# Kernel tuning notes

Hardware: AMD Instinct MI355X
Metric: run time of the kernel (lower is better)

## Reference

```python
import jax, jax.numpy as jnp
import numpy as np

B, S, SV = 4, 2048, 50
QF = KF = VF = E = 1024
SCALE = np.float32(np.power(KF, 0.5))


def setup_inputs() -> dict:
    key = jax.random.key(0)
    ks = jax.random.split(key, 8)
    s = 0.02
    return {
        "Q": jax.random.normal(ks[0], (B, S, QF), dtype=jnp.float32),
        "K": jax.random.normal(ks[1], (B, S, KF), dtype=jnp.float32),
        "V": jax.random.normal(ks[2], (B, SV, VF), dtype=jnp.float32),
        # weights stored [in, out] so forward is x @ W (== torch Linear with weight.T)
        "W_Q": jax.random.normal(ks[3], (QF, E), dtype=jnp.float32) * s,
        "W_K": jax.random.normal(ks[4], (KF, E), dtype=jnp.float32) * s,
        "W_v": jax.random.normal(ks[5], (E, E), dtype=jnp.float32) * s,
        "W_vq": jax.random.normal(ks[6], (SV, E), dtype=jnp.float32) * s,
        "W_vk": jax.random.normal(ks[7], (SV, E), dtype=jnp.float32) * s,
    }


def reference(Q, K, V, W_Q, W_K, W_v, W_vq, W_vk):
    # mode == 'mode2', dropout=None (inference path)
    q = jnp.tanh(Q) @ W_Q          # [B,S,E]
    k = jnp.tanh(K) @ W_K          # [B,S,E]
    v = jnp.tanh(V) @ W_v          # [B,SV,E]

    qk = jnp.einsum('bse,bte->bst', q, k) / SCALE   # [B,S,S]
    vq = jnp.einsum('bse,bve->bsv', q, v) / SCALE   # [B,S,SV]
    vk = jnp.einsum('bse,bve->bsv', k, v) / SCALE   # [B,S,SV]

    f = jax.nn.softmax(qk, axis=-1)                 # [B,S,S]
    g = 1.0 - f

    q2 = jnp.einsum('bst,bte->bse', f, q) + vq @ W_vq
    k2 = jnp.einsum('bst,bte->bse', g, k) + vk @ W_vk

    Q_out = jnp.einsum('bst,bte->bse', f, q2)
    K_out = jnp.einsum('bst,bte->bse', g, k2)
    return (Q_out, K_out, f)
```

## Files before the change

### kernel.cpp

```cpp
#include <hip/hip_runtime.h>
#include <cstdint>
#include <cstddef>

typedef __bf16 bf16_t;
typedef __bf16 bf16x4 __attribute__((ext_vector_type(4)));
typedef __bf16 bf16x8 __attribute__((ext_vector_type(8)));
typedef float floatx4 __attribute__((ext_vector_type(4)));

#define B_ 4
#define S_ 2048
#define E_ 1024
#define SV_ 50
#define SVP_ 64
#define BSE_ ((long)B_ * S_ * E_)

__device__ __forceinline__ void async_copy16(const bf16_t* g, bf16_t* l) {
  __builtin_amdgcn_global_load_lds(
      (const __attribute__((address_space(1))) void*)g,
      (__attribute__((address_space(3))) void*)l, 16, 0, 0);
}

__global__ __launch_bounds__(256) void tanh2_k(const float* __restrict__ Q,
                                               const float* __restrict__ Kin,
                                               bf16_t* __restrict__ out) {
  long i4 = ((long)blockIdx.x * 256 + threadIdx.x) * 4;
  const long n = (long)B_ * S_ * E_;
  const float* src = (i4 < n) ? (Q + i4) : (Kin + (i4 - n));
  float4 x = *(const float4*)src;
  bf16x4 o;
  o[0] = (bf16_t)tanhf(x.x);
  o[1] = (bf16_t)tanhf(x.y);
  o[2] = (bf16_t)tanhf(x.z);
  o[3] = (bf16_t)tanhf(x.w);
  *(bf16x4*)&out[i4] = o;
}

__global__ __launch_bounds__(256) void tanh_vpad_k(const float* __restrict__ V,
                                                   bf16_t* __restrict__ out) {
  int i = blockIdx.x * 256 + threadIdx.x;
  int e = i & 1023, r = (i >> 10) & 63, b = i >> 16;
  float v = 0.f;
  if (r < SV_) v = tanhf(V[((long)(b * SV_ + r) << 10) + e]);
  out[i] = (bf16_t)v;
}

__global__ __launch_bounds__(256) void transp_cast3_k(const float* __restrict__ W0,
                                                      const float* __restrict__ W1,
                                                      const float* __restrict__ W2,
                                                      bf16_t* __restrict__ out,
                                                      int K, int N, int Kp) {
  __shared__ float tile[32][33];
  const float* W = (blockIdx.z == 0) ? W0 : (blockIdx.z == 1) ? W1 : W2;
  bf16_t* o = out + (long)blockIdx.z * N * Kp;
  int k0 = blockIdx.y * 32, n0 = blockIdx.x * 32;
  int tx = threadIdx.x, ty = threadIdx.y;
#pragma unroll
  for (int s2 = 0; s2 < 4; ++s2) {
    int kk = ty + s2 * 8;
    float v = 0.f;
    if (k0 + kk < K && n0 + tx < N) v = W[(long)(k0 + kk) * N + n0 + tx];
    tile[kk][tx] = v;
  }
  __syncthreads();
#pragma unroll
  for (int s2 = 0; s2 < 4; ++s2) {
    int nn = ty + s2 * 8;
    if (n0 + nn < N && k0 + tx < Kp)
      o[(long)(n0 + nn) * Kp + k0 + tx] = (bf16_t)tile[tx][nn];
  }
}

__global__ __launch_bounds__(256) void transp2_bf16_k(const bf16_t* __restrict__ in,
                                                      long selIn, long inRow,
                                                      long inBatch,
                                                      bf16_t* __restrict__ out,
                                                      long selOut, long outRow,
                                                      long outBatch,
                                                      float* __restrict__ csum) {
  __shared__ bf16_t tile[32][33];
  __shared__ float cs[8][32];
  int r0 = blockIdx.y * 32, c0 = blockIdx.x * 32;
  int tx = threadIdx.x, ty = threadIdx.y;
  int half = blockIdx.z & 1, bz = blockIdx.z >> 1;
  long ib = (long)bz * inBatch + (long)half * selIn;
  long ob = (long)bz * outBatch + (long)half * selOut;
  float ps = 0.f;
#pragma unroll
  for (int s2 = 0; s2 < 4; ++s2) {
    bf16_t v = in[ib + (long)(r0 + ty + s2 * 8) * inRow + c0 + tx];
    tile[ty + s2 * 8][tx] = v;
    ps += (float)v;
  }
  cs[ty][tx] = ps;
  __syncthreads();
#pragma unroll
  for (int s2 = 0; s2 < 4; ++s2)
    out[ob + (long)(c0 + ty + s2 * 8) * outRow + r0 + tx] = tile[tx][ty + s2 * 8];
  if (csum && half == 1 && ty == 0) {
    float s = 0.f;
#pragma unroll
    for (int c = 0; c < 8; ++c) s += cs[c][tx];
    atomicAdd(&csum[(long)bz * E_ + c0 + tx], s);
  }
}

__global__ __launch_bounds__(256) void softmax_row_k(bf16_t* __restrict__ fb,
                                                     float* __restrict__ Fout) {
  long off = ((long)blockIdx.y * S_ + blockIdx.x) * S_;
  int t = threadIdx.x;
  bf16x8 xb = *(const bf16x8*)&fb[off + 8 * t];
  float x[8];
#pragma unroll
  for (int i = 0; i < 8; ++i) x[i] = (float)xb[i];
  float mx = fmaxf(fmaxf(fmaxf(x[0], x[1]), fmaxf(x[2], x[3])),
                   fmaxf(fmaxf(x[4], x[5]), fmaxf(x[6], x[7])));
#pragma unroll
  for (int s = 32; s >= 1; s >>= 1) mx = fmaxf(mx, __shfl_xor(mx, s));
  __shared__ float red[4];
  int wv = t >> 6;
  if ((t & 63) == 0) red[wv] = mx;
  __syncthreads();
  mx = fmaxf(fmaxf(red[0], red[1]), fmaxf(red[2], red[3]));
  float e[8];
  float sum = 0.f;
#pragma unroll
  for (int i = 0; i < 8; ++i) {
    e[i] = __expf(x[i] - mx);
    sum += e[i];
  }
#pragma unroll
  for (int s = 32; s >= 1; s >>= 1) sum += __shfl_xor(sum, s);
  __shared__ float red2[4];
  if ((t & 63) == 0) red2[wv] = sum;
  __syncthreads();
  float inv = 1.0f / ((red2[0] + red2[1]) + (red2[2] + red2[3]));
  bf16x8 ob;
#pragma unroll
  for (int i = 0; i < 8; ++i) {
    e[i] *= inv;
    ob[i] = (bf16_t)e[i];
  }
  *(float4*)&Fout[off + 8 * t] = make_float4(e[0], e[1], e[2], e[3]);
  *(float4*)&Fout[off + 8 * t + 4] = make_float4(e[4], e[5], e[6], e[7]);
  *(bf16x8*)&fb[off + 8 * t] = ob;
}

__global__ __launch_bounds__(256) void gemm_vqk_k(const bf16_t* __restrict__ qkb,
                                                  const bf16_t* __restrict__ vb,
                                                  bf16_t* __restrict__ vqkf) {
  __shared__ __align__(16) bf16_t As[64 * 64];
  __shared__ __align__(16) bf16_t Bs[64 * 64];
  const int zz = blockIdx.z;
  const int sel = zz >> 2;
  const int b = zz & 3;
  const bf16_t* Ab = qkb + (long)sel * BSE_ + (long)b * S_ * E_;
  const bf16_t* Bb = vb + (long)b * SVP_ * E_;
  bf16_t* outB = vqkf + ((long)b * 2 + sel) * ((long)S_ * SVP_);
  const int t = threadIdx.x;
  const int lane = t & 63;
  const int wave = t >> 6;
  const int wm = (wave & 1) * 32;
  const int wn = (wave >> 1) * 32;
  const long rowBase = (long)blockIdx.y * 64;

  floatx4 acc[2][2];
#pragma unroll
  for (int i = 0; i < 2; ++i)
#pragma unroll
    for (int j = 0; j < 2; ++j) acc[i][j] = {0.f, 0.f, 0.f, 0.f};

  const int sr = t >> 3;
  const int sc = (t & 7) * 8;
  for (int k0 = 0; k0 < E_; k0 += 64) {
#pragma unroll
    for (int p = 0; p < 2; ++p) {
      int r = p * 32 + sr;
      *(uint4*)&As[r * 64 + sc] = *(const uint4*)&Ab[(rowBase + r) * E_ + k0 + sc];
      *(uint4*)&Bs[r * 64 + sc] = *(const uint4*)&Bb[(long)r * E_ + k0 + sc];
    }
    __syncthreads();
#pragma unroll
    for (int ks = 0; ks < 64; ks += 32) {
      const int fr = lane & 15;
      const int fk = ks + ((lane >> 4) << 3);
      bf16x8 a0 = *(const bf16x8*)&As[(wm + fr) * 64 + fk];
      bf16x8 a1 = *(const bf16x8*)&As[(wm + 16 + fr) * 64 + fk];
      bf16x8 b0 = *(const bf16x8*)&Bs[(wn + fr) * 64 + fk];
      bf16x8 b1 = *(const bf16x8*)&Bs[(wn + 16 + fr) * 64 + fk];
      acc[0][0] = __builtin_amdgcn_mfma_f32_16x16x32_bf16(a0, b0, acc[0][0], 0, 0, 0);
      acc[0][1] = __builtin_amdgcn_mfma_f32_16x16x32_bf16(a0, b1, acc[0][1], 0, 0, 0);
      acc[1][0] = __builtin_amdgcn_mfma_f32_16x16x32_bf16(a1, b0, acc[1][0], 0, 0, 0);
      acc[1][1] = __builtin_amdgcn_mfma_f32_16x16x32_bf16(a1, b1, acc[1][1], 0, 0, 0);
    }
    __syncthreads();
  }

  const int cr = lane & 15;
  const int rq = (lane >> 4) * 4;
  const float alpha = sel ? -1.f / 32.f : 1.f / 32.f;
#pragma unroll
  for (int i = 0; i < 2; ++i)
#pragma unroll
    for (int j = 0; j < 2; ++j)
#pragma unroll
      for (int r = 0; r < 4; ++r) {
        long row = rowBase + wm + i * 16 + rq + r;
        int col = wn + j * 16 + cr;
        outB[row * SVP_ + col] = (bf16_t)(alpha * acc[i][j][r]);
      }
}

__global__ __launch_bounds__(512, 2) void gemm256_k(
    const bf16_t* __restrict__ A1, long sA1,
    const bf16_t* __restrict__ B1, long sB1,
    int N, int K1,
    const bf16_t* __restrict__ A2q, const bf16_t* __restrict__ A2k, long sA2,
    const bf16_t* __restrict__ B2,
    float alpha, int negSplit, const float* __restrict__ colVec, long sV,
    float* __restrict__ outFa, bf16_t* __restrict__ outBa, int lda, long sOa,
    float* __restrict__ outFb, bf16_t* __restrict__ outBb, int ldb, long sOb,
    int capZ, int capM) {
  __shared__ __align__(16) bf16_t As[2 * 256 * 64];
  __shared__ __align__(16) bf16_t Bs[2 * 256 * 64];
  const int t = threadIdx.x;
  const int lane = t & 63;
  const int wave = t >> 6;
  const int wr = wave >> 2;
  const int wc = wave & 3;
  const long b = blockIdx.z;
  const long rowBase = (long)blockIdx.y * 256;
  const long colBase = (long)blockIdx.x * 256;
  if ((int)b >= capZ && rowBase >= capM) return;
  const bf16_t* Ab = A1 + b * sA1;
  const bf16_t* Bb = B1 + b * sB1;

  floatx4 acc[8][4];
#pragma unroll
  for (int i = 0; i < 8; ++i)
#pragma unroll
    for (int j = 0; j < 4; ++j) acc[i][j] = {0.f, 0.f, 0.f, 0.f};

  const int srow = t >> 3;
  const int sch = (t & 7) ^ (srow & 7);
  const bf16_t* aG = Ab + (rowBase + srow) * (long)K1 + sch * 8;
  const bf16_t* bG = Bb + (colBase + srow) * (long)K1 + sch * 8;
  const bf16_t* A2 = A2q ? ((colBase >= negSplit) ? A2k : A2q) : nullptr;
  const bf16_t* a2G = A2 ? A2 + b * sA2 + (rowBase + srow) * 64 + sch * 8 : aG;
  const bf16_t* b2G = A2 ? B2 + (colBase + srow) * 64 + sch * 8 : bG;
  const int ldsW = (wave * 8) * 64;

  const int fr = lane & 15;
  const int hi = lane >> 4;
  const int swz = (hi ^ (fr & 7)) * 8;
  int aoff[8], boff[4];
#pragma unroll
  for (int i = 0; i < 8; ++i) aoff[i] = (wr * 128 + i * 16 + fr) * 64 + swz;
#pragma unroll
  for (int j = 0; j < 4; ++j) boff[j] = (wc * 64 + j * 16 + fr) * 64 + swz;

  const int nK1 = K1 >> 6;
  const int nt = nK1 + (A2q ? 1 : 0);

  auto stageTile = [&](int buf, int kt) {
    const int bo = buf * (256 * 64);
    bf16_t* la = &As[bo + ldsW];
    bf16_t* lb = &Bs[bo + ldsW];
    if (kt < nK1) {
      const long k0 = (long)kt * 64;
#pragma unroll
      for (int h = 0; h < 4; ++h) {
        async_copy16(aG + (long)(h * 64) * K1 + k0, la + h * 64 * 64);
        async_copy16(bG + (long)(h * 64) * K1 + k0, lb + h * 64 * 64);
      }
    } else {
#pragma unroll
      for (int h = 0; h < 4; ++h) {
        async_copy16(a2G + h * 64 * 64, la + h * 64 * 64);
        async_copy16(b2G + h * 64 * 64, lb + h * 64 * 64);
      }
    }
  };

  stageTile(0, 0);

  for (int kt = 0; kt < nt; ++kt) {
    const int bo = (kt & 1) * (256 * 64);
    bf16x8 a0l[4], a0h[4], a1l[4], a1h[4], b0l[2], b0h[2], b1l[2], b1h[2];

    if (kt + 1 < nt) {
      stageTile((kt + 1) & 1, kt + 1);
      asm volatile("s_waitcnt vmcnt(8)" ::: "memory");
    } else {
      asm volatile("s_waitcnt vmcnt(0)" ::: "memory");
    }
    __builtin_amdgcn_s_barrier();
    __builtin_amdgcn_sched_barrier(0);
#pragma unroll
    for (int i = 0; i < 4; ++i) {
      a0l[i] = *(const bf16x8*)&As[bo + aoff[i]];
      a0h[i] = *(const bf16x8*)&As[bo + (aoff[i] ^ 32)];
    }
#pragma unroll
    for (int j = 0; j < 2; ++j) {
      b0l[j] = *(const bf16x8*)&Bs[bo + boff[j]];
      b0h[j] = *(const bf16x8*)&Bs[bo + (boff[j] ^ 32)];
    }
    __builtin_amdgcn_s_setprio(1);
#pragma unroll
    for (int i = 0; i < 4; ++i)
#pragma unroll
      for (int j = 0; j < 2; ++j) {
        acc[i][j] = __builtin_amdgcn_mfma_f32_16x16x32_bf16(a0l[i], b0l[j], acc[i][j], 0, 0, 0);
        acc[i][j] = __builtin_amdgcn_mfma_f32_16x16x32_bf16(a0h[i], b0h[j], acc[i][j], 0, 0, 0);
      }
    __builtin_amdgcn_s_setprio(0);
    __builtin_amdgcn_sched_barrier(0);

    __builtin_amdgcn_s_barrier();
    __builtin_amdgcn_sched_barrier(0);
#pragma unroll
    for (int j = 0; j < 2; ++j) {
      b1l[j] = *(const bf16x8*)&Bs[bo + boff[j + 2]];
      b1h[j] = *(const bf16x8*)&Bs[bo + (boff[j + 2] ^ 32)];
    }
    __builtin_amdgcn_s_setprio(1);
#pragma unroll
    for (int i = 0; i < 4; ++i)
#pragma unroll
      for (int j = 0; j < 2; ++j) {
        acc[i][j + 2] = __builtin_amdgcn_mfma_f32_16x16x32_bf16(a0l[i], b1l[j], acc[i][j + 2], 0, 0, 0);
        acc[i][j + 2] = __builtin_amdgcn_mfma_f32_16x16x32_bf16(a0h[i], b1h[j], acc[i][j + 2], 0, 0, 0);
      }
    __builtin_amdgcn_s_setprio(0);
    __builtin_amdgcn_sched_barrier(0);

    __builtin_amdgcn_s_barrier();
    __builtin_amdgcn_sched_barrier(0);
#pragma unroll
    for (int i = 0; i < 4; ++i) {
      a1l[i] = *(const bf16x8*)&As[bo + aoff[i + 4]];
      a1h[i] = *(const bf16x8*)&As[bo + (aoff[i + 4] ^ 32)];
    }
    __builtin_amdgcn_s_setprio(1);
#pragma unroll
    for (int i = 0; i < 4; ++i)
#pragma unroll
      for (int j = 0; j < 2; ++j) {
        acc[i + 4][j + 2] = __builtin_amdgcn_mfma_f32_16x16x32_bf16(a1l[i], b1l[j], acc[i + 4][j + 2], 0, 0, 0);
        acc[i + 4][j + 2] = __builtin_amdgcn_mfma_f32_16x16x32_bf16(a1h[i], b1h[j], acc[i + 4][j + 2], 0, 0, 0);
      }
    __builtin_amdgcn_s_setprio(0);
    __builtin_amdgcn_sched_barrier(0);

    __builtin_amdgcn_s_barrier();
    __builtin_amdgcn_sched_barrier(0);
    __builtin_amdgcn_s_setprio(1);
#pragma unroll
    for (int i = 0; i < 4; ++i)
#pragma unroll
      for (int j = 0; j < 2; ++j) {
        acc[i + 4][j] = __builtin_amdgcn_mfma_f32_16x16x32_bf16(a1l[i], b0l[j], acc[i + 4][j], 0, 0, 0);
        acc[i + 4][j] = __builtin_amdgcn_mfma_f32_16x16x32_bf16(a1h[i], b0h[j], acc[i + 4][j], 0, 0, 0);
      }
    __builtin_amdgcn_s_setprio(0);
    __builtin_amdgcn_sched_barrier(0);
  }

  const int cr = lane & 15;
  const int rq = hi * 4;
  const bool neg = (colBase >= negSplit);
  const float* cv = colVec ? (colVec + b * sV + (neg ? colBase - negSplit : colBase))
                           : nullptr;
  float* oF = neg ? outFb : outFa;
  bf16_t* oB = neg ? outBb : outBa;
  const int ld = neg ? ldb : lda;
  const long sO = neg ? sOb : sOa;
  const long cb0 = neg ? (long)(colBase - negSplit) : colBase;
#pragma unroll
  for (int i = 0; i < 8; ++i)
#pragma unroll
    for (int j = 0; j < 4; ++j)
#pragma unroll
      for (int r = 0; r < 4; ++r) {
        long row = rowBase + wr * 128 + i * 16 + rq + r;
        int c = wc * 64 + j * 16 + cr;
        float v = alpha * acc[i][j][r];
        if (neg) v = cv[c] - v;
        long o = b * sO + row * (long)ld + cb0 + c;
        if (oF) oF[o] = v;
        if (oB) oB[o] = (bf16_t)v;
      }
}

extern "C" void kernel_launch(void* const* d_in, const int* in_sizes, int n_in,
                              void* d_out, int out_size, void* d_ws, size_t ws_size,
                              hipStream_t stream) {
  const float* Q = (const float*)d_in[0];
  const float* Kin = (const float*)d_in[1];
  const float* V = (const float*)d_in[2];
  const float* W_Q = (const float*)d_in[3];
  const float* W_K = (const float*)d_in[4];
  const float* W_v = (const float*)d_in[5];
  const float* W_vq = (const float*)d_in[6];
  const float* W_vk = (const float*)d_in[7];

  float* Qout = (float*)d_out;
  float* Kout = Qout + (long)B_ * S_ * E_;
  float* Fout = Kout + (long)B_ * S_ * E_;

  char* w = (char*)d_ws;
  auto alloc = [&](size_t bytes) {
    char* p = w;
    w += (bytes + 255) & ~(size_t)255;
    return p;
  };
  const long BSE = BSE_;
  bf16_t* WQKt = (bf16_t*)alloc((size_t)2 * 2 * E_ * E_);
  bf16_t* WVt = (bf16_t*)alloc((size_t)2 * E_ * E_);
  bf16_t* Wv2T = (bf16_t*)alloc((size_t)2 * 2 * E_ * SVP_);
  bf16_t* QtKt = (bf16_t*)alloc((size_t)2 * 2 * BSE);
  bf16_t* Vt = (bf16_t*)alloc((size_t)2 * B_ * SVP_ * E_);
  bf16_t* qkb = (bf16_t*)alloc((size_t)2 * 2 * BSE);
  bf16_t* vb = (bf16_t*)alloc((size_t)2 * B_ * SVP_ * E_);
  bf16_t* qkT = (bf16_t*)alloc((size_t)2 * (long)B_ * 2 * E_ * S_);
  bf16_t* fb = (bf16_t*)alloc((size_t)2 * (long)B_ * S_ * S_);
  bf16_t* vqkf = (bf16_t*)alloc((size_t)2 * (long)B_ * 2 * S_ * SVP_);
  bf16_t* q2k2 = (bf16_t*)alloc((size_t)2 * (long)B_ * S_ * 2 * E_);
  bf16_t* q2k2T = (bf16_t*)alloc((size_t)2 * (long)B_ * 2 * E_ * S_);
  float* ck = (float*)alloc((size_t)4 * B_ * E_);
  float* ck2 = (float*)alloc((size_t)4 * B_ * E_);

  bf16_t* qb = qkb;
  bf16_t* kb = qkb + BSE;

  dim3 blk256(256);
  dim3 blk512(512);
  dim3 blk32x8(32, 8);

  hipMemsetAsync(ck, 0, (size_t)2 * 4 * B_ * E_, stream);

  transp_cast3_k<<<dim3(32, 32, 3), blk32x8, 0, stream>>>(W_Q, W_K, W_v, WQKt,
                                                          E_, E_, E_);
  transp_cast3_k<<<dim3(32, 2, 2), blk32x8, 0, stream>>>(W_vq, W_vk, W_vq, Wv2T,
                                                         SV_, E_, SVP_);

  tanh2_k<<<dim3((unsigned)(2 * BSE / 1024)), blk256, 0, stream>>>(Q, Kin, QtKt);
  tanh_vpad_k<<<dim3(B_ * SVP_ * E_ / 256), blk256, 0, stream>>>(V, Vt);

  gemm256_k<<<dim3(E_ / 256, B_ * S_ / 256, 3), blk512, 0, stream>>>(
      QtKt, BSE, WQKt, (long)E_ * E_, E_, E_,
      nullptr, nullptr, 0, nullptr, 1.f, E_, nullptr, 0,
      nullptr, qkb, E_, BSE, nullptr, nullptr, 0, 0,
      2, B_ * SVP_);

  transp2_bf16_k<<<dim3(E_ / 32, S_ / 32, 2 * B_), blk32x8, 0, stream>>>(
      qkb, BSE, E_, (long)S_ * E_, qkT, (long)E_ * S_, S_, (long)2 * E_ * S_, ck);

  gemm256_k<<<dim3(S_ / 256, S_ / 256, B_), blk512, 0, stream>>>(
      qb, (long)S_ * E_, kb, (long)S_ * E_, S_, E_,
      nullptr, nullptr, 0, nullptr, 1.f / 32.f, S_, nullptr, 0,
      nullptr, fb, S_, (long)S_ * S_, nullptr, nullptr, 0, 0,
      9999, 0);
  softmax_row_k<<<dim3(S_, B_), blk256, 0, stream>>>(fb, Fout);

  gemm_vqk_k<<<dim3(1, S_ / 64, 2 * B_), blk256, 0, stream>>>(qkb, vb, vqkf);

  gemm256_k<<<dim3(2 * E_ / 256, S_ / 256, B_), blk512, 0, stream>>>(
      fb, (long)S_ * S_, qkT, (long)2 * E_ * S_, 2 * E_, S_,
      vqkf, vqkf + (long)S_ * SVP_, (long)2 * S_ * SVP_, Wv2T,
      1.f, E_, ck, E_,
      nullptr, q2k2, 2 * E_, (long)S_ * 2 * E_,
      nullptr, q2k2 + E_, 2 * E_, (long)S_ * 2 * E_,
      9999, 0);

  transp2_bf16_k<<<dim3(E_ / 32, S_ / 32, 2 * B_), blk32x8, 0, stream>>>(
      q2k2, E_, 2 * E_, (long)S_ * 2 * E_, q2k2T, (long)E_ * S_, S_,
      (long)2 * E_ * S_, ck2);

  gemm256_k<<<dim3(2 * E_ / 256, S_ / 256, B_), blk512, 0, stream>>>(
      fb, (long)S_ * S_, q2k2T, (long)2 * E_ * S_, 2 * E_, S_,
      nullptr, nullptr, 0, nullptr,
      1.f, E_, ck2, E_,
      Qout, nullptr, E_, (long)S_ * E_,
      Kout, nullptr, E_, (long)S_ * E_,
      9999, 0);
}
```

Baseline: 572.9 us.

## Interleave global-to-LDS staging into GEMM compute phases with finer vmcnt waits

Splits each k-tile's async global-to-LDS copy into four units (A and B halves) and issues them between the four MFMA phases of the main loop. Part of tile kt+2 is prefetched into the buffer being freed, so loads are spread across the iteration instead of bursting at its start. Partial vmcnt waits (2, 8, 10) replace the single wait. This aims to smooth memory traffic and hide load latency, but the fine-grained buffer reuse depends on exact barrier and wait counts and risks subtle races.

```diff
diff --git a/kernel.cpp b/kernel.cpp
--- a/kernel.cpp
+++ b/kernel.cpp
@@ -18,6 +18,17 @@
   __builtin_amdgcn_global_load_lds(
       (const __attribute__((address_space(1))) void*)g,
       (__attribute__((address_space(3))) void*)l, 16, 0, 0);
+}
+
+__device__ __forceinline__ void vm_wait(int n) {
+  if (n == 0)
+    asm volatile("s_waitcnt vmcnt(0)" ::: "memory");
+  else if (n == 2)
+    asm volatile("s_waitcnt vmcnt(2)" ::: "memory");
+  else if (n == 8)
+    asm volatile("s_waitcnt vmcnt(8)" ::: "memory");
+  else
+    asm volatile("s_waitcnt vmcnt(10)" ::: "memory");
 }
 
 __global__ __launch_bounds__(256) void tanh2_k(const float* __restrict__ Q,
@@ -261,38 +272,44 @@
   const int nK1 = K1 >> 6;
   const int nt = nK1 + (A2q ? 1 : 0);
 
-  auto stageTile = [&](int buf, int kt) {
+  auto stageUnit = [&](int u, int buf, int kt) {
     const int bo = buf * (256 * 64);
-    bf16_t* la = &As[bo + ldsW];
-    bf16_t* lb = &Bs[bo + ldsW];
+    int h0, h1;
+    bool isA;
+    if (u == 0) { isA = true;  h0 = 0; h1 = 2; }
+    else if (u == 1) { isA = false; h0 = 0; h1 = 1; }
+    else if (u == 2) { isA = false; h0 = 2; h1 = 3; }
+    else { isA = true;  h0 = 1; h1 = 3; }
+    bf16_t* l = isA ? &As[bo + ldsW] : &Bs[bo + ldsW];
     if (kt < nK1) {
       const long k0 = (long)kt * 64;
-#pragma unroll
-      for (int h = 0; h < 4; ++h) {
-        async_copy16(aG + (long)(h * 64) * K1 + k0, la + h * 64 * 64);
-        async_copy16(bG + (long)(h * 64) * K1 + k0, lb + h * 64 * 64);
-      }
+      const bf16_t* g = isA ? aG : bG;
+      async_copy16(g + (long)(h0 * 64) * K1 + k0, l + h0 * 64 * 64);
+      async_copy16(g + (long)(h1 * 64) * K1 + k0, l + h1 * 64 * 64);
     } else {
-#pragma unroll
-      for (int h = 0; h < 4; ++h) {
-        async_copy16(a2G + h * 64 * 64, la + h * 64 * 64);
-        async_copy16(b2G + h * 64 * 64, lb + h * 64 * 64);
-      }
+      const bf16_t* g = isA ? a2G : b2G;
+      async_copy16(g + h0 * 64 * 64, l + h0 * 64 * 64);
+      async_copy16(g + h1 * 64 * 64, l + h1 * 64 * 64);
     }
   };
 
-  stageTile(0, 0);
+  stageUnit(0, 0, 0);
+  stageUnit(1, 0, 0);
+  stageUnit(2, 0, 0);
+  stageUnit(3, 0, 0);
+  if (nt > 1) {
+    stageUnit(0, 1, 1);
+    stageUnit(1, 1, 1);
+  }
 
   for (int kt = 0; kt < nt; ++kt) {
     const int bo = (kt & 1) * (256 * 64);
+    const int v1 = (kt + 1 < nt) ? 8 : 2;
+    const int v3 = (kt + 2 < nt) ? 10 : ((kt + 1 < nt) ? 8 : 0);
     bf16x8 a0l[4], a0h[4], a1l[4], a1h[4], b0l[2], b0h[2], b1l[2], b1h[2];
 
-    if (kt + 1 < nt) {
-      stageTile((kt + 1) & 1, kt + 1);
-      asm volatile("s_waitcnt vmcnt(8)" ::: "memory");
-    } else {
-      asm volatile("s_waitcnt vmcnt(0)" ::: "memory");
-    }
+    if (kt + 1 < nt) stageUnit(2, (kt + 1) & 1, kt + 1);
+    vm_wait(v1);
     __builtin_amdgcn_s_barrier();
     __builtin_amdgcn_sched_barrier(0);
 #pragma unroll
@@ -316,6 +333,7 @@
     __builtin_amdgcn_s_setprio(0);
     __builtin_amdgcn_sched_barrier(0);
 
+    if (kt + 1 < nt) stageUnit(3, (kt + 1) & 1, kt + 1);
     __builtin_amdgcn_s_barrier();
     __builtin_amdgcn_sched_barrier(0);
 #pragma unroll
@@ -334,6 +352,8 @@
     __builtin_amdgcn_s_setprio(0);
     __builtin_amdgcn_sched_barrier(0);
 
+    if (kt + 2 < nt) stageUnit(0, (kt + 2) & 1, kt + 2);
+    vm_wait(v3);
     __builtin_amdgcn_s_barrier();
     __builtin_amdgcn_sched_barrier(0);
 #pragma unroll
@@ -352,6 +372,7 @@
     __builtin_amdgcn_s_setprio(0);
     __builtin_amdgcn_sched_barrier(0);
 
+    if (kt + 2 < nt) stageUnit(1, (kt + 2) & 1, kt + 2);
     __builtin_amdgcn_s_barrier();
     __builtin_amdgcn_sched_barrier(0);
     __builtin_amdgcn_s_setprio(1);
```

New measurement: 570.8 us. Within noise of the previous version (-0.4%).
